# Performance work log

Hardware: AMD Instinct MI355X
Metric: run time of the kernel (lower is better)

Reference implementation:

```python
import jax, jax.numpy as jnp
import numpy as np

NEG = -1e9


def _ln(x, g, b):
    m = x.mean(-1, keepdims=True)
    v = ((x - m) ** 2).mean(-1, keepdims=True)
    return (x - m) / jnp.sqrt(v + 1e-5) * g + b


def _block(single, pair, single_mask, pair_mask,
           pa_ln_g, pa_ln_b, pa_wqkv, pa_wg, pa_wout,
           pt_ln_g, pt_ln_b, pt_w1, pt_b1, pt_w2, pt_b2,
           sa_ln_g, sa_ln_b, sa_wq, sa_wkv, sa_wb, sa_wout,
           st_ln_g, st_ln_b, st_w1, st_b1, st_w2, st_b2):
    B, L, _, D = pair.shape
    H = sa_wb.shape[1]
    hd = D // H
    scale = 1.0 / jnp.sqrt(jnp.asarray(hd, dtype=pair.dtype))
    # ---- PairUpdate: PairAttention over L*L pseudo-tokens ----
    z = _ln(pair, pa_ln_g, pa_ln_b)                       # [B,L,L,D]
    N = L * L
    qkv = (z @ pa_wqkv).reshape(B, N, 3, H, hd)
    q = qkv[:, :, 0].transpose(0, 2, 1, 3)                # [B,H,N,hd]
    k = qkv[:, :, 1].transpose(0, 2, 1, 3)
    v = qkv[:, :, 2].transpose(0, 2, 1, 3)
    attn = jnp.einsum('bhid,bhjd->bhij', q, k) * scale    # [B,H,N,N]
    pm = pair_mask.reshape(B, 1, N)
    m = pm[:, :, :, None] * pm[:, :, None, :]             # [B,1,N,N]
    attn = jnp.where(m > 0, attn, NEG)
    attn = jax.nn.softmax(attn, axis=-1)
    out = jnp.einsum('bhij,bhjd->bhid', attn, v)          # [B,H,N,hd]
    out = out.transpose(0, 2, 1, 3).reshape(B, L, L, D)
    g = jax.nn.sigmoid(z @ pa_wg)
    out = (out @ pa_wout) * g * pair_mask[..., None]
    pair = pair + out
    t = _ln(pair, pt_ln_g, pt_ln_b)
    t = jax.nn.relu(t @ pt_w1 + pt_b1) @ pt_w2 + pt_b2
    pair = pair + t * pair_mask[..., None]
    # ---- SingleUpdate: AttentionPairBias ----
    s = _ln(single, sa_ln_g, sa_ln_b)                     # [B,L,D]
    q = (s @ sa_wq).reshape(B, L, H, hd)
    kv = (s @ sa_wkv).reshape(B, L, 2, H, hd)
    k2, v2 = kv[:, :, 0], kv[:, :, 1]
    attn = jnp.einsum('bihd,bjhd->bhij', q, k2) * scale   # [B,H,L,L]
    bias = (pair @ sa_wb).transpose(0, 3, 1, 2)           # [B,H,L,L]
    attn = attn + bias
    sm = single_mask[:, None, None, :]
    attn = jnp.where(sm > 0, attn, NEG)
    attn = jax.nn.softmax(attn, axis=-1)
    out = jnp.einsum('bhij,bjhd->bihd', attn, v2).reshape(B, L, D)
    single = single + (out @ sa_wout) * single_mask[..., None]
    # single transition
    t = _ln(single, st_ln_g, st_ln_b)
    t = jax.nn.relu(t @ st_w1 + st_b1) @ st_w2 + st_b2
    single = single + t * single_mask[..., None]
    return single, pair


def setup_inputs() -> dict:
    key = jax.random.key(0)
    B, L, D, H = 1, 64, 144, 8
    ks = iter(jax.random.split(key, 40))
    def nrm(shape, scale=0.02):
        return jax.random.normal(next(ks), shape, dtype=jnp.float32) * scale
    sm = jnp.ones((B, L), jnp.float32).at[:, L - 8:].set(0.0)
    pm = sm[:, :, None] * sm[:, None, :]
    return dict(
        single=jax.random.normal(next(ks), (B, L, D), jnp.float32),
        pair=jax.random.normal(next(ks), (B, L, L, D), jnp.float32),
        single_mask=sm,
        pair_mask=pm,
        pa_ln_g=jnp.ones((D,), jnp.float32), pa_ln_b=jnp.zeros((D,), jnp.float32),
        pa_wqkv=nrm((D, 3 * D)), pa_wg=nrm((D, D)), pa_wout=nrm((D, D)),
        pt_ln_g=jnp.ones((D,), jnp.float32), pt_ln_b=jnp.zeros((D,), jnp.float32),
        pt_w1=nrm((D, 4 * D)), pt_b1=jnp.zeros((4 * D,), jnp.float32),
        pt_w2=nrm((4 * D, D)), pt_b2=jnp.zeros((D,), jnp.float32),
        sa_ln_g=jnp.ones((D,), jnp.float32), sa_ln_b=jnp.zeros((D,), jnp.float32),
        sa_wq=nrm((D, D)), sa_wkv=nrm((D, 2 * D)), sa_wb=nrm((D, H)), sa_wout=nrm((D, D)),
        st_ln_g=jnp.ones((D,), jnp.float32), st_ln_b=jnp.zeros((D,), jnp.float32),
        st_w1=nrm((D, 4 * D)), st_b1=jnp.zeros((4 * D,), jnp.float32),
        st_w2=nrm((4 * D, D)), st_b2=jnp.zeros((D,), jnp.float32),
    )


def reference(single, pair, single_mask, pair_mask,
              pa_ln_g, pa_ln_b, pa_wqkv, pa_wg, pa_wout,
              pt_ln_g, pt_ln_b, pt_w1, pt_b1, pt_w2, pt_b2,
              sa_ln_g, sa_ln_b, sa_wq, sa_wkv, sa_wb, sa_wout,
              st_ln_g, st_ln_b, st_w1, st_b1, st_w2, st_b2):
    return _block(single, pair, single_mask, pair_mask,
                  pa_ln_g, pa_ln_b, pa_wqkv, pa_wg, pa_wout,
                  pt_ln_g, pt_ln_b, pt_w1, pt_b1, pt_w2, pt_b2,
                  sa_ln_g, sa_ln_b, sa_wq, sa_wkv, sa_wb, sa_wout,
                  st_ln_g, st_ln_b, st_w1, st_b1, st_w2, st_b2)
```

## Files before the change

kernel.cpp:

```cpp
#include <hip/hip_runtime.h>
#include <hip/hip_bf16.h>

typedef __hip_bfloat16 bf16;
typedef __attribute__((ext_vector_type(8))) short short8;
typedef __attribute__((ext_vector_type(16))) float floatx16;

__device__ __forceinline__ float tof(bf16 x){ return __bfloat162float(x); }
__device__ __forceinline__ float bflo(unsigned u){ return __uint_as_float(u<<16); }
__device__ __forceinline__ float bfhi(unsigned u){ return __uint_as_float(u & 0xFFFF0000u); }
__device__ __forceinline__ float ldT(const void* p, long i, bool isf){
  return isf ? ((const float*)p)[i] : tof(((const bf16*)p)[i]);
}
__device__ __forceinline__ void stT(void* p, long i, bool isf, float v){
  if (isf) ((float*)p)[i] = v; else ((bf16*)p)[i] = __float2bfloat16(v);
}

#define LL 64
#define DD 144
#define NN 4096
#define HH 8
#define HDIM 18
#define SCALE 0.23570226039551584f
#define LOG2E 1.4426950408889634f

__global__ __launch_bounds__(256) void prep_weights(const unsigned* __restrict__ smaskw,
    int* __restrict__ dflag,
    const void* __restrict__ wqkv, const void* __restrict__ wg,
    const void* __restrict__ wout, const void* __restrict__ w1, const void* __restrict__ w2,
    const void* __restrict__ swq, const void* __restrict__ swkv,
    const void* __restrict__ swout, const void* __restrict__ sw1, const void* __restrict__ sw2,
    bf16* __restrict__ F1, bf16* __restrict__ Fout, bf16* __restrict__ Fw1,
    bf16* __restrict__ Fw2, bf16* __restrict__ Fs1, bf16* __restrict__ Wtswout,
    bf16* __restrict__ Wtst1, bf16* __restrict__ Wtst2){
  bool isf = (smaskw[0] == 0x3F800000u);
  if (blockIdx.x==0 && threadIdx.x==0) dflag[0] = isf ? 4 : 2;
  long t = (long)blockIdx.x*256 + threadIdx.x;
  if (t < 82944){
    int j=t&7, lane=(int)((t>>3)&63); long tk=t>>9; int ks=tk%9, tile=tk/9;
    int col=tile*32+(lane&31); int k=ks*16+(lane>>5)*8+j;
    float v = (col<432)? ldT(wqkv,(long)k*432+col,isf) : ldT(wg,(long)k*144+(col-432),isf);
    F1[t]=__float2bfloat16(v); return;
  } t -= 82944;
  if (t < 23040){
    int j=t&7, lane=(int)((t>>3)&63); long tk=t>>9; int ks=tk%9, tile=tk/9;
    int col=tile*32+(lane&31); if (col>143) col=143;
    int k=ks*16+(lane>>5)*8+j;
    Fout[t]=__float2bfloat16(ldT(wout,(long)k*144+col,isf)); return;
  } t -= 23040;
  if (t < 82944){
    int j=t&7, lane=(int)((t>>3)&63); long tk=t>>9; int ks=tk%9, tile=tk/9;
    int col=tile*32+(lane&31); int k=ks*16+(lane>>5)*8+j;
    Fw1[t]=__float2bfloat16(ldT(w1,(long)k*576+col,isf)); return;
  } t -= 82944;
  if (t < 92160){
    int j=t&7, lane=(int)((t>>3)&63); long tk=t>>9; int ks=tk%36, tile=tk/36;
    int col=tile*32+(lane&31); if (col>143) col=143;
    int k=ks*16+(lane>>5)*8+j;
    Fw2[t]=__float2bfloat16(ldT(w2,(long)k*144+col,isf)); return;
  } t -= 92160;
  if (t < 64512){
    int j=t&7, lane=(int)((t>>3)&63); long tk=t>>9; int ks=tk%9, tile=tk/9;
    int col=tile*32+(lane&31); if (col>431) col=431;
    int k=ks*16+(lane>>5)*8+j;
    float v = (col<144)? ldT(swq,(long)k*144+col,isf) : ldT(swkv,(long)k*288+(col-144),isf);
    Fs1[t]=__float2bfloat16(v); return;
  } t -= 64512;
  if (t < 20736){ int c=t/144,k=t-(long)c*144; Wtswout[t]=__float2bfloat16(ldT(swout,(long)k*144+c,isf)); return; }
  t -= 20736;
  if (t < 82944){ int c=t/144,k=t-(long)c*144; Wtst1[t]=__float2bfloat16(ldT(sw1,(long)k*576+c,isf)); return; }
  t -= 82944;
  if (t < 82944){ int c=t/576,k=t-(long)c*576; Wtst2[t]=__float2bfloat16(ldT(sw2,(long)k*144+c,isf)); return; }
}

__global__ __launch_bounds__(256) void ln_rows(const int* __restrict__ df,
    const void* __restrict__ xv,
    const void* __restrict__ gv, const void* __restrict__ bv,
    bf16* __restrict__ out){
  bool isf = (df[0]==4);
  int row = blockIdx.x*4 + (threadIdx.x>>6);
  int lane = threadIdx.x & 63;
  long base = (long)row*DD;
  float e0 = ldT(xv,base+lane,isf);
  float e1 = ldT(xv,base+lane+64,isf);
  float e2 = (lane<16) ? ldT(xv,base+lane+128,isf) : 0.f;
  float s = e0+e1+e2;
  #pragma unroll
  for (int o=32;o;o>>=1) s += __shfl_xor(s,o);
  float mean = s*(1.f/144.f);
  float d0=e0-mean, d1=e1-mean, d2=(lane<16)?(e2-mean):0.f;
  float v = d0*d0+d1*d1+d2*d2;
  #pragma unroll
  for (int o=32;o;o>>=1) v += __shfl_xor(v,o);
  float rstd = rsqrtf(v*(1.f/144.f)+1e-5f);
  out[base+lane]    = __float2bfloat16(d0*rstd*ldT(gv,lane,isf)    + ldT(bv,lane,isf));
  out[base+lane+64] = __float2bfloat16(d1*rstd*ldT(gv,lane+64,isf) + ldT(bv,lane+64,isf));
  if (lane<16)
    out[base+lane+128] = __float2bfloat16(d2*rstd*ldT(gv,lane+128,isf) + ldT(bv,lane+128,isf));
}

__global__ __launch_bounds__(256) void gemm_fused1(const int* __restrict__ df,
    const bf16* __restrict__ z, const bf16* __restrict__ F1,
    const void* __restrict__ pmask,
    bf16* __restrict__ Qb, bf16* __restrict__ Kf, bf16* __restrict__ Vf,
    bf16* __restrict__ gbuf){
  __shared__ short As[64*152];
  bool isf = df[0]==4;
  int row0 = blockIdx.y*64, col0 = blockIdx.x*64;
  int tid=threadIdx.x, lane=tid&63, l31=lane&31, w=tid>>6, wr=w>>1, wc=w&1;
  int g=(lane>>5)*8;
  for (int t=tid; t<64*72; t+=256){
    int m = t/72, dw = t%72;
    ((unsigned*)As)[m*76+dw] = ((const unsigned*)(z + (size_t)(row0+m)*144))[dw];
  }
  __syncthreads();
  int tile = blockIdx.x*2 + wc;
  const short8* wf = (const short8*)F1;
  floatx16 acc;
  #pragma unroll
  for (int i=0;i<16;i++) acc[i]=0.f;
  #pragma unroll
  for (int ks=0; ks<9; ks++){
    short8 af = *(const short8*)&As[(l31+32*wr)*152 + ks*16 + g];
    acc = __builtin_amdgcn_mfma_f32_32x32x16_bf16(af, wf[(tile*9+ks)*64+lane], acc, 0,0,0);
  }
  int col = col0 + wc*32 + l31;
  #pragma unroll
  for (int r=0;r<16;r++){
    int row = row0 + 32*wr + (r&3)+8*(r>>2)+4*(lane>>5);
    if (col < 144){
      int hh = col/18, d = col - hh*18;
      Qb[((size_t)hh*NN+row)*32 + d] = __float2bfloat16(acc[r]*(SCALE*LOG2E));
    } else if (col < 288){
      int c2 = col-144, hh = c2/18, d = c2 - hh*18;
      int f = d>>4, rem = d&15, gs = rem>>3, j = rem&7;
      Kf[((((size_t)hh*128 + (row>>5))*2 + f)*64 + gs*32 + (row&31))*8 + j]
        = __float2bfloat16(acc[r]);
    } else if (col < 432){
      int c2 = col-288, hh = c2/18, d = c2 - hh*18;
      float pm = (ldT(pmask,row,isf)>0.f)?1.f:0.f;
      int kin = row&31, f = kin>>4, k15 = kin&15;
      int gs = (k15>>2)&1, j = (k15&3) | (((k15>>3)&1)<<2);
      Vf[((((size_t)hh*128 + (row>>5))*2 + f)*64 + gs*32 + d)*8 + j]
        = __float2bfloat16(acc[r]*pm);
    } else {
      int c2 = col-432;
      float gt = 1.f/(1.f+__expf(fminf(-acc[r],30.f)));
      gbuf[(size_t)row*DD+c2] = __float2bfloat16(gt);
    }
  }
  if (blockIdx.x==0){
    for (int t=threadIdx.x; t<64*8*7; t+=256){
      int n = row0 + t/56; int rem = t%56; int hh = rem/7, dw = rem%7 + 9;
      ((unsigned*)(Qb + ((size_t)hh*NN+n)*32))[dw] = 0;
    }
    for (int t=threadIdx.x; t<64*8; t+=256){
      int n = row0 + (t>>3), hh = t&7;
      float pm = (ldT(pmask,n,isf)>0.f)?1.f:0.f;
      int kin = n&31, f = kin>>4, k15 = kin&15;
      int gs = (k15>>2)&1, j = (k15&3) | (((k15>>3)&1)<<2);
      Vf[((((size_t)hh*128 + (n>>5))*2 + f)*64 + gs*32 + 18)*8 + j] = __float2bfloat16(pm);
    }
  }
}

__global__ __launch_bounds__(256) void pair_attn_mfma(const int* __restrict__ df,
    const bf16* __restrict__ Qb, const bf16* __restrict__ Kf,
    const bf16* __restrict__ Vf, bf16* __restrict__ aob){
  __shared__ float Comb[4][32][20];
  int h = blockIdx.x >> 7, qt = blockIdx.x & 127;
  int tid = threadIdx.x;
  int w = tid >> 6, lane = tid & 63;
  int l31 = lane & 31, gsel = lane>>5;

  const unsigned* qp = (const unsigned*)(Qb + ((size_t)h*NN + qt*32 + l31)*32);
  short8 qf0, qf1;
  #pragma unroll
  for (int j=0;j<4;j++) ((unsigned*)&qf0)[j] = qp[gsel*4+j];
  #pragma unroll
  for (int j=0;j<4;j++) ((unsigned*)&qf1)[j] = qp[8+gsel*4+j];

  floatx16 o;
  #pragma unroll
  for (int i=0;i<16;i++) o[i]=0.f;

  const short8* kf8 = (const short8*)Kf + (size_t)h*16384;
  const short8* vf8 = (const short8*)Vf + (size_t)h*16384;
  int c0 = w*32;

  short8 af0 = kf8[(c0*2+0)*64 + lane];
  short8 af1 = kf8[(c0*2+1)*64 + lane];
  short8 av0 = vf8[(c0*2+0)*64 + lane];
  short8 av1 = vf8[(c0*2+1)*64 + lane];

  for (int cc=0; cc<32; cc++){
    int cn = c0 + (cc<31 ? cc+1 : 31);
    short8 naf0 = kf8[(cn*2+0)*64 + lane];
    short8 naf1 = kf8[(cn*2+1)*64 + lane];
    short8 nav0 = vf8[(cn*2+0)*64 + lane];
    short8 nav1 = vf8[(cn*2+1)*64 + lane];

    floatx16 s;
    #pragma unroll
    for (int i=0;i<16;i++) s[i]=0.f;
    s = __builtin_amdgcn_mfma_f32_32x32x16_bf16(af0, qf0, s, 0,0,0);
    s = __builtin_amdgcn_mfma_f32_32x32x16_bf16(af1, qf1, s, 0,0,0);

    short8 P1, P2;
    #pragma unroll
    for (int j=0;j<4;j++){
      unsigned e0 = __float_as_uint(__builtin_amdgcn_exp2f(s[2*j]));
      unsigned e1 = __float_as_uint(__builtin_amdgcn_exp2f(s[2*j+1]));
      ((unsigned*)&P1)[j] = (e0>>16) | (e1 & 0xFFFF0000u);
      unsigned e2 = __float_as_uint(__builtin_amdgcn_exp2f(s[8+2*j]));
      unsigned e3 = __float_as_uint(__builtin_amdgcn_exp2f(s[9+2*j]));
      ((unsigned*)&P2)[j] = (e2>>16) | (e3 & 0xFFFF0000u);
    }

    o = __builtin_amdgcn_mfma_f32_32x32x16_bf16(av0, P1, o, 0,0,0);
    o = __builtin_amdgcn_mfma_f32_32x32x16_bf16(av1, P2, o, 0,0,0);

    af0=naf0; af1=naf1; av0=nav0; av1=nav1;
  }

  #pragma unroll
  for (int r=0;r<16;r++){
    int d = (r&3) + 8*(r>>2) + 4*gsel;
    if (d < 20) Comb[w][l31][d] = o[r];
  }
  __syncthreads();
  for (int t=tid; t<32*HDIM; t+=256){
    int q = t/HDIM, d = t-q*HDIM;
    float num = Comb[0][q][d]+Comb[1][q][d]+Comb[2][q][d]+Comb[3][q][d];
    float den = Comb[0][q][18]+Comb[1][q][18]+Comb[2][q][18]+Comb[3][q][18];
    aob[(size_t)(qt*32+q)*DD + h*HDIM + d] = __float2bfloat16(num/fmaxf(den,1e-20f));
  }
}

__global__ __launch_bounds__(512) void pair_tail(const int* __restrict__ df,
    const bf16* __restrict__ aob, const bf16* __restrict__ gbuf,
    const void* __restrict__ pairv, const void* __restrict__ pmaskv,
    const bf16* __restrict__ Fout, const void* __restrict__ ptln_g, const void* __restrict__ ptln_b,
    const bf16* __restrict__ Fw1, const void* __restrict__ b1v,
    const bf16* __restrict__ Fw2, const void* __restrict__ b2v,
    const void* __restrict__ wb, void* __restrict__ outP, long outOff,
    float* __restrict__ biasb){
  __shared__ __align__(16) char smem[16384];
  float* p1  = (float*)smem;
  short* ts  = (short*)(smem + 4608);
  short* hh_ = (short*)(smem + 7040);
  float* outv = (float*)(smem + 7040);

  bool isf = df[0]==4;
  int tid=threadIdx.x, lane=tid&63, l31=lane&31, gsel=lane>>5, g=gsel*8;
  int w=tid>>6;
  int lrow = l31 & 7;
  int r0 = blockIdx.x*8;
  const short8* foutf = (const short8*)Fout;
  const short8* fw1f  = (const short8*)Fw1;
  const short8* fw2f  = (const short8*)Fw2;

  for (int t=tid; t<8*72; t+=512){
    int m=t/72, dw=t%72;
    ((unsigned*)ts)[m*76+dw] = ((const unsigned*)(aob + (size_t)(r0+m)*144))[dw];
  }
  __syncthreads();

  for (int tile=w; tile<5; tile+=8){
    int c0=tile*32;
    floatx16 acc;
    #pragma unroll
    for (int i=0;i<16;i++) acc[i]=0.f;
    #pragma unroll
    for (int ks=0; ks<9; ks++){
      short8 af = *(const short8*)&ts[lrow*152 + ks*16 + g];
      acc = __builtin_amdgcn_mfma_f32_32x32x16_bf16(af, foutf[(tile*9+ks)*64+lane], acc, 0,0,0);
    }
    if (c0+l31 < 144){
      #pragma unroll
      for (int r=0;r<16;r++){
        int row=(r&3)+8*(r>>2)+4*gsel;
        if (row<8) p1[row*144 + c0+l31] = acc[r];
      }
    }
  }
  __syncthreads();
  for (int t=tid; t<8*144; t+=512){
    int row=t/144; int col=t-row*144;
    long gidx=(long)(r0+row)*144 + col;
    float pm = (ldT(pmaskv, r0+row, isf)>0.f)?1.f:0.f;
    p1[t] = ldT(pairv,gidx,isf) + p1[t]*tof(gbuf[gidx])*pm;
  }
  __syncthreads();
  if (w < 8){
    int rr = w;
    float e0=p1[rr*144+lane], e1=p1[rr*144+lane+64], e2=(lane<16)?p1[rr*144+lane+128]:0.f;
    float s=e0+e1+e2;
    #pragma unroll
    for (int o=32;o;o>>=1) s += __shfl_xor(s,o);
    float mean=s*(1.f/144.f);
    float d0=e0-mean, d1=e1-mean, d2=(lane<16)?(e2-mean):0.f;
    float v=d0*d0+d1*d1+d2*d2;
    #pragma unroll
    for (int o=32;o;o>>=1) v += __shfl_xor(v,o);
    float rstd=rsqrtf(v*(1.f/144.f)+1e-5f);
    bf16 h0 = __float2bfloat16(d0*rstd*ldT(ptln_g,lane,isf)    + ldT(ptln_b,lane,isf));
    bf16 h1 = __float2bfloat16(d1*rstd*ldT(ptln_g,lane+64,isf) + ldT(ptln_b,lane+64,isf));
    ts[rr*152+lane]    = *reinterpret_cast<short*>(&h0);
    ts[rr*152+lane+64] = *reinterpret_cast<short*>(&h1);
    if (lane<16){
      bf16 h2 = __float2bfloat16(d2*rstd*ldT(ptln_g,lane+128,isf) + ldT(ptln_b,lane+128,isf));
      ts[rr*152+lane+128] = *reinterpret_cast<short*>(&h2);
    }
  }
  __syncthreads();
  for (int tile=w; tile<18; tile+=8){
    int c0=tile*32, colB=c0+l31;
    floatx16 acc;
    #pragma unroll
    for (int i=0;i<16;i++) acc[i]=0.f;
    #pragma unroll
    for (int ks=0; ks<9; ks++){
      short8 af = *(const short8*)&ts[lrow*152 + ks*16 + g];
      acc = __builtin_amdgcn_mfma_f32_32x32x16_bf16(af, fw1f[(tile*9+ks)*64+lane], acc, 0,0,0);
    }
    float bb = ldT(b1v,colB,isf);
    #pragma unroll
    for (int r=0;r<16;r++){
      int row=(r&3)+8*(r>>2)+4*gsel;
      if (row<8){
        bf16 hv = __float2bfloat16(fmaxf(acc[r]+bb,0.f));
        hh_[row*584 + colB] = *reinterpret_cast<short*>(&hv);
      }
    }
  }
  __syncthreads();
  floatx16 fin; int fc0 = -1;
  for (int tile=w; tile<5; tile+=8){
    int c0=tile*32;
    int colB=c0+l31; if (colB>143) colB=143;
    floatx16 acc;
    #pragma unroll
    for (int i=0;i<16;i++) acc[i]=0.f;
    #pragma unroll
    for (int ks=0; ks<36; ks++){
      short8 af = *(const short8*)&hh_[lrow*584 + ks*16 + g];
      acc = __builtin_amdgcn_mfma_f32_32x32x16_bf16(af, fw2f[(tile*36+ks)*64+lane], acc, 0,0,0);
    }
    float bb = ldT(b2v,colB,isf);
    #pragma unroll
    for (int r=0;r<16;r++){
      int row=(r&3)+8*(r>>2)+4*gsel;
      float val = 0.f;
      if (row<8){
        float pm = (ldT(pmaskv, r0+row, isf)>0.f)?1.f:0.f;
        val = p1[row*144 + colB] + (acc[r]+bb)*pm;
        if (c0+l31 < 144)
          stT(outP, outOff + (long)(r0+row)*144 + c0+l31, isf, val);
      }
      fin[r]=val;
    }
    fc0 = c0;
  }
  __syncthreads();
  if (fc0 >= 0 && fc0+l31 < 144){
    #pragma unroll
    for (int r=0;r<16;r++){
      int row=(r&3)+8*(r>>2)+4*gsel;
      if (row<8) outv[row*144 + fc0+l31] = fin[r];
    }
  }
  __syncthreads();
  {
    int n = tid>>3, hb = tid&7;
    if (n < 8){
      float acc=0.f;
      #pragma unroll 4
      for (int k=0;k<144;k++) acc += outv[n*144+k]*ldT(wb,k*8+hb,isf);
      biasb[(size_t)(r0+n)*8+hb]=acc;
    }
  }
}

__global__ __launch_bounds__(256) void gemm_s1(const int* __restrict__ df,
    const void* __restrict__ single, const void* __restrict__ g, const void* __restrict__ b,
    const bf16* __restrict__ Fs1,
    bf16* __restrict__ q_sb, bf16* __restrict__ kv_sb){
  __shared__ short As[64*152];
  bool isf = df[0]==4;
  int tid=threadIdx.x, lane=tid&63, l31=lane&31, w=tid>>6, wr=w>>1, wc=w&1;
  int gg=(lane>>5)*8;
  for (int rr=w; rr<64; rr+=4){
    long base=(long)rr*DD;
    float e0=ldT(single,base+lane,isf), e1=ldT(single,base+lane+64,isf);
    float e2=(lane<16)?ldT(single,base+lane+128,isf):0.f;
    float s=e0+e1+e2;
    #pragma unroll
    for (int o=32;o;o>>=1) s += __shfl_xor(s,o);
    float mean=s*(1.f/144.f);
    float d0=e0-mean, d1=e1-mean, d2=(lane<16)?(e2-mean):0.f;
    float v=d0*d0+d1*d1+d2*d2;
    #pragma unroll
    for (int o=32;o;o>>=1) v += __shfl_xor(v,o);
    float rstd=rsqrtf(v*(1.f/144.f)+1e-5f);
    bf16 h0=__float2bfloat16(d0*rstd*ldT(g,lane,isf)+ldT(b,lane,isf));
    bf16 h1=__float2bfloat16(d1*rstd*ldT(g,lane+64,isf)+ldT(b,lane+64,isf));
    As[rr*152+lane]=*reinterpret_cast<short*>(&h0);
    As[rr*152+lane+64]=*reinterpret_cast<short*>(&h1);
    if (lane<16){
      bf16 h2=__float2bfloat16(d2*rstd*ldT(g,lane+128,isf)+ldT(b,lane+128,isf));
      As[rr*152+lane+128]=*reinterpret_cast<short*>(&h2);
    }
  }
  __syncthreads();
  int tile = blockIdx.x*2 + wc;
  const short8* wf = (const short8*)Fs1;
  floatx16 acc;
  #pragma unroll
  for (int i=0;i<16;i++) acc[i]=0.f;
  #pragma unroll
  for (int ks=0; ks<9; ks++){
    short8 af = *(const short8*)&As[(l31+32*wr)*152 + ks*16 + gg];
    acc = __builtin_amdgcn_mfma_f32_32x32x16_bf16(af, wf[(tile*9+ks)*64+lane], acc, 0,0,0);
  }
  int col = tile*32 + l31;
  if (col < 432){
    #pragma unroll
    for (int r=0;r<16;r++){
      int row = 32*wr + (r&3)+8*(r>>2)+4*(lane>>5);
      if (col<144) q_sb[(size_t)row*DD+col] = __float2bfloat16(acc[r]);
      else kv_sb[(size_t)row*288+(col-144)] = __float2bfloat16(acc[r]);
    }
  }
}

__global__ __launch_bounds__(256) void single_tail(const int* __restrict__ df,
    const void* __restrict__ single, const bf16* __restrict__ q_sb,
    const bf16* __restrict__ kv_sb, const float* __restrict__ biasb,
    const void* __restrict__ smask, const bf16* __restrict__ Wtswout,
    const void* __restrict__ stln_g, const void* __restrict__ stln_b,
    const bf16* __restrict__ Wtst1, const void* __restrict__ st_b1,
    const bf16* __restrict__ Wtst2, const void* __restrict__ st_b2,
    void* __restrict__ outS){
  bool isf = df[0]==4;
  __shared__ short kvs[64*288];
  __shared__ float pexp[8][64];
  __shared__ float tot[8];
  __shared__ float bb[512];
  __shared__ float qs[DD], as_[DD], s1[DD], tss[DD], hs[576];
  int n = blockIdx.x, tid = threadIdx.x;
  for (int t=tid; t<64*144; t+=256)
    ((unsigned*)kvs)[t] = ((const unsigned*)kv_sb)[t];
  if (tid<DD) qs[tid] = tof(q_sb[(size_t)n*DD+tid]);
  for (int t=tid; t<512; t+=256) bb[t] = biasb[(size_t)n*512 + t];
  __syncthreads();
  #pragma unroll
  for (int pp=0; pp<2; pp++){
    int pi = tid + pp*256;
    int h = pi>>6, j = pi&63;
    const short* kr = &kvs[j*288 + h*HDIM];
    float s=0.f;
    #pragma unroll
    for (int d=0;d<HDIM;d++){
      unsigned u = ((unsigned)(unsigned short)kr[d])<<16;
      s += qs[h*HDIM+d]*__uint_as_float(u);
    }
    s = fminf(s*SCALE + bb[j*8+h], 30.f);
    pexp[h][j] = (ldT(smask,j,isf)>0.f) ? __expf(s) : 0.f;
  }
  __syncthreads();
  if (tid<8){
    float t2=0.f;
    #pragma unroll 4
    for (int j=0;j<64;j++) t2 += pexp[tid][j];
    tot[tid] = fmaxf(t2,1e-20f);
  }
  __syncthreads();
  if (tid<DD){
    int h = tid/HDIM, d = tid - h*HDIM;
    float acc=0.f;
    #pragma unroll 4
    for (int j=0;j<64;j++){
      unsigned u = ((unsigned)(unsigned short)kvs[j*288 + 144 + h*HDIM + d])<<16;
      acc += pexp[h][j]*__uint_as_float(u);
    }
    as_[tid] = acc/tot[h];
  }
  __syncthreads();
  float sm = ldT(smask,n,isf);
  if (tid<DD){
    const unsigned* wr = (const unsigned*)(Wtswout + (size_t)tid*DD);
    float a=0.f;
    #pragma unroll 4
    for (int kw=0; kw<72; kw++){ unsigned u = wr[kw]; a += as_[2*kw]*bflo(u) + as_[2*kw+1]*bfhi(u); }
    s1[tid] = ldT(single,(long)n*DD+tid,isf) + a*sm;
  }
  __syncthreads();
  __shared__ float mr[2];
  if (tid < 64){
    float e0 = s1[tid], e1 = s1[tid+64], e2 = (tid<16)?s1[tid+128]:0.f;
    float s = e0+e1+e2;
    #pragma unroll
    for (int o=32;o;o>>=1) s += __shfl_xor(s,o);
    float mean = s*(1.f/144.f);
    float d0=e0-mean, d1=e1-mean, d2=(tid<16)?(e2-mean):0.f;
    float v = d0*d0+d1*d1+d2*d2;
    #pragma unroll
    for (int o=32;o;o>>=1) v += __shfl_xor(v,o);
    if (tid==0){ mr[0]=mean; mr[1]=rsqrtf(v*(1.f/144.f)+1e-5f); }
  }
  __syncthreads();
  if (tid<DD) tss[tid] = (s1[tid]-mr[0])*mr[1]*ldT(stln_g,tid,isf) + ldT(stln_b,tid,isf);
  __syncthreads();
  for (int c=tid;c<576;c+=256){
    const unsigned* wr = (const unsigned*)(Wtst1 + (size_t)c*DD);
    float a=ldT(st_b1,c,isf);
    #pragma unroll 4
    for (int kw=0; kw<72; kw++){ unsigned u = wr[kw]; a += tss[2*kw]*bflo(u) + tss[2*kw+1]*bfhi(u); }
    hs[c]=fmaxf(a,0.f);
  }
  __syncthreads();
  if (tid<DD){
    const unsigned* wr = (const unsigned*)(Wtst2 + (size_t)tid*576);
    float a=ldT(st_b2,tid,isf);
    #pragma unroll 4
    for (int kw=0; kw<288; kw++){ unsigned u = wr[kw]; a += hs[2*kw]*bflo(u) + hs[2*kw+1]*bfhi(u); }
    stT(outS,(long)n*DD+tid,isf, s1[tid] + a*sm);
  }
}

extern "C" void kernel_launch(void* const* d_in, const int* in_sizes, int n_in,
                              void* d_out, int out_size, void* d_ws, size_t ws_size,
                              hipStream_t stream) {
  char* wsb = (char*)d_ws;
  int*   dflag = (int*)wsb;
  bf16*  F1     = (bf16*)(wsb + 16);
  bf16*  Fout   = F1 + 82944;
  bf16*  Fw1    = Fout + 23040;
  bf16*  Fw2    = Fw1 + 82944;
  bf16*  Fs1    = Fw2 + 92160;
  bf16*  Wtswout= Fs1 + 64512;
  bf16*  Wtst1  = Wtswout + 20736;
  bf16*  Wtst2  = Wtst1 + 82944;
  bf16*  Qb   = Wtst2 + 82944;
  bf16*  Kf   = Qb + (size_t)HH*NN*32;
  bf16*  Vf   = Kf + (size_t)HH*131072;
  bf16*  gbuf = Vf + (size_t)HH*131072;
  bf16*  z    = gbuf + (size_t)NN*DD;
  bf16*  aob  = z + (size_t)NN*DD;
  float* biasb= (float*)(aob + (size_t)NN*DD);
  bf16*  q_sb = (bf16*)(biasb + NN*8);
  bf16*  kv_sb= q_sb + LL*DD;

  const long OUTP_OFF = (long)LL*DD;

  prep_weights<<<2079,256,0,stream>>>((const unsigned*)d_in[2], dflag,
      d_in[6], d_in[7], d_in[8], d_in[11], d_in[13],
      d_in[17], d_in[18], d_in[20], d_in[23], d_in[25],
      F1, Fout, Fw1, Fw2, Fs1, Wtswout, Wtst1, Wtst2);

  ln_rows<<<NN/4,256,0,stream>>>(dflag, d_in[1], d_in[4], d_in[5], z);
  gemm_fused1<<<dim3(9,64),256,0,stream>>>(dflag, z, F1, d_in[3], Qb, Kf, Vf, gbuf);
  pair_attn_mfma<<<1024,256,0,stream>>>(dflag, Qb, Kf, Vf, aob);
  pair_tail<<<512,512,0,stream>>>(dflag, aob, gbuf, d_in[1], d_in[3],
                                  Fout, d_in[9], d_in[10], Fw1, d_in[12],
                                  Fw2, d_in[14], d_in[19], d_out, OUTP_OFF, biasb);

  gemm_s1<<<dim3(7,1),256,0,stream>>>(dflag, d_in[0], d_in[15], d_in[16], Fs1, q_sb, kv_sb);
  single_tail<<<LL,256,0,stream>>>(dflag, d_in[0], q_sb, kv_sb, biasb, d_in[2],
                                   Wtswout, d_in[21], d_in[22], Wtst1, d_in[24],
                                   Wtst2, d_in[26], d_out);
  (void)in_sizes; (void)n_in; (void)out_size; (void)ws_size;
}
```

Baseline: 239.6 us.

## Fuse pair LayerNorm into QKV GEMM, fuse single path, reorder attention blocks

Folds the pair LayerNorm into the QKV/gate GEMM's shared-memory staging, so the separate ln_rows launch and the z buffer round-trip disappear. The single-track LN+QKV GEMM is merged into the single tail kernel: each of the 64 blocks recomputes the full 64-row projection locally instead of reading from a separate launch. Pair attention block indexing now interleaves heads across consecutive blocks, and MFMA sections are wrapped with s_setprio. The fusions save two launches and a global round-trip but add redundant work: the 9 column blocks each redo the LN on their rows, and every single-track block recomputes the same GEMM.

```diff
diff --git a/kernel.cpp b/kernel.cpp
--- a/kernel.cpp
+++ b/kernel.cpp
@@ -72,34 +72,9 @@
   if (t < 82944){ int c=t/576,k=t-(long)c*576; Wtst2[t]=__float2bfloat16(ldT(sw2,(long)k*144+c,isf)); return; }
 }
 
-__global__ __launch_bounds__(256) void ln_rows(const int* __restrict__ df,
-    const void* __restrict__ xv,
-    const void* __restrict__ gv, const void* __restrict__ bv,
-    bf16* __restrict__ out){
-  bool isf = (df[0]==4);
-  int row = blockIdx.x*4 + (threadIdx.x>>6);
-  int lane = threadIdx.x & 63;
-  long base = (long)row*DD;
-  float e0 = ldT(xv,base+lane,isf);
-  float e1 = ldT(xv,base+lane+64,isf);
-  float e2 = (lane<16) ? ldT(xv,base+lane+128,isf) : 0.f;
-  float s = e0+e1+e2;
-  #pragma unroll
-  for (int o=32;o;o>>=1) s += __shfl_xor(s,o);
-  float mean = s*(1.f/144.f);
-  float d0=e0-mean, d1=e1-mean, d2=(lane<16)?(e2-mean):0.f;
-  float v = d0*d0+d1*d1+d2*d2;
-  #pragma unroll
-  for (int o=32;o;o>>=1) v += __shfl_xor(v,o);
-  float rstd = rsqrtf(v*(1.f/144.f)+1e-5f);
-  out[base+lane]    = __float2bfloat16(d0*rstd*ldT(gv,lane,isf)    + ldT(bv,lane,isf));
-  out[base+lane+64] = __float2bfloat16(d1*rstd*ldT(gv,lane+64,isf) + ldT(bv,lane+64,isf));
-  if (lane<16)
-    out[base+lane+128] = __float2bfloat16(d2*rstd*ldT(gv,lane+128,isf) + ldT(bv,lane+128,isf));
-}
-
 __global__ __launch_bounds__(256) void gemm_fused1(const int* __restrict__ df,
-    const bf16* __restrict__ z, const bf16* __restrict__ F1,
+    const void* __restrict__ pairv, const void* __restrict__ lng, const void* __restrict__ lnb,
+    const bf16* __restrict__ F1,
     const void* __restrict__ pmask,
     bf16* __restrict__ Qb, bf16* __restrict__ Kf, bf16* __restrict__ Vf,
     bf16* __restrict__ gbuf){
@@ -108,9 +83,27 @@
   int row0 = blockIdx.y*64, col0 = blockIdx.x*64;
   int tid=threadIdx.x, lane=tid&63, l31=lane&31, w=tid>>6, wr=w>>1, wc=w&1;
   int g=(lane>>5)*8;
-  for (int t=tid; t<64*72; t+=256){
-    int m = t/72, dw = t%72;
-    ((unsigned*)As)[m*76+dw] = ((const unsigned*)(z + (size_t)(row0+m)*144))[dw];
+  for (int rr=w; rr<64; rr+=4){
+    long base=(long)(row0+rr)*DD;
+    float e0=ldT(pairv,base+lane,isf), e1=ldT(pairv,base+lane+64,isf);
+    float e2=(lane<16)?ldT(pairv,base+lane+128,isf):0.f;
+    float s=e0+e1+e2;
+    #pragma unroll
+    for (int o=32;o;o>>=1) s += __shfl_xor(s,o);
+    float mean=s*(1.f/144.f);
+    float d0=e0-mean, d1=e1-mean, d2=(lane<16)?(e2-mean):0.f;
+    float v=d0*d0+d1*d1+d2*d2;
+    #pragma unroll
+    for (int o=32;o;o>>=1) v += __shfl_xor(v,o);
+    float rstd=rsqrtf(v*(1.f/144.f)+1e-5f);
+    bf16 h0=__float2bfloat16(d0*rstd*ldT(lng,lane,isf)+ldT(lnb,lane,isf));
+    bf16 h1=__float2bfloat16(d1*rstd*ldT(lng,lane+64,isf)+ldT(lnb,lane+64,isf));
+    As[rr*152+lane]=*reinterpret_cast<short*>(&h0);
+    As[rr*152+lane+64]=*reinterpret_cast<short*>(&h1);
+    if (lane<16){
+      bf16 h2=__float2bfloat16(d2*rstd*ldT(lng,lane+128,isf)+ldT(lnb,lane+128,isf));
+      As[rr*152+lane+128]=*reinterpret_cast<short*>(&h2);
+    }
   }
   __syncthreads();
   int tile = blockIdx.x*2 + wc;
@@ -167,7 +160,7 @@
     const bf16* __restrict__ Qb, const bf16* __restrict__ Kf,
     const bf16* __restrict__ Vf, bf16* __restrict__ aob){
   __shared__ float Comb[4][32][20];
-  int h = blockIdx.x >> 7, qt = blockIdx.x & 127;
+  int h = blockIdx.x & 7, qt = blockIdx.x >> 3;
   int tid = threadIdx.x;
   int w = tid >> 6, lane = tid & 63;
   int l31 = lane & 31, gsel = lane>>5;
@@ -202,8 +195,10 @@
     floatx16 s;
     #pragma unroll
     for (int i=0;i<16;i++) s[i]=0.f;
+    __builtin_amdgcn_s_setprio(1);
     s = __builtin_amdgcn_mfma_f32_32x32x16_bf16(af0, qf0, s, 0,0,0);
     s = __builtin_amdgcn_mfma_f32_32x32x16_bf16(af1, qf1, s, 0,0,0);
+    __builtin_amdgcn_s_setprio(0);
 
     short8 P1, P2;
     #pragma unroll
@@ -216,8 +211,10 @@
       ((unsigned*)&P2)[j] = (e2>>16) | (e3 & 0xFFFF0000u);
     }
 
+    __builtin_amdgcn_s_setprio(1);
     o = __builtin_amdgcn_mfma_f32_32x32x16_bf16(av0, P1, o, 0,0,0);
     o = __builtin_amdgcn_mfma_f32_32x32x16_bf16(av1, P2, o, 0,0,0);
+    __builtin_amdgcn_s_setprio(0);
 
     af0=naf0; af1=naf1; av0=nav0; av1=nav1;
   }
@@ -381,78 +378,78 @@
   }
 }
 
-__global__ __launch_bounds__(256) void gemm_s1(const int* __restrict__ df,
-    const void* __restrict__ single, const void* __restrict__ g, const void* __restrict__ b,
-    const bf16* __restrict__ Fs1,
-    bf16* __restrict__ q_sb, bf16* __restrict__ kv_sb){
-  __shared__ short As[64*152];
-  bool isf = df[0]==4;
-  int tid=threadIdx.x, lane=tid&63, l31=lane&31, w=tid>>6, wr=w>>1, wc=w&1;
-  int gg=(lane>>5)*8;
-  for (int rr=w; rr<64; rr+=4){
-    long base=(long)rr*DD;
-    float e0=ldT(single,base+lane,isf), e1=ldT(single,base+lane+64,isf);
-    float e2=(lane<16)?ldT(single,base+lane+128,isf):0.f;
-    float s=e0+e1+e2;
-    #pragma unroll
-    for (int o=32;o;o>>=1) s += __shfl_xor(s,o);
-    float mean=s*(1.f/144.f);
-    float d0=e0-mean, d1=e1-mean, d2=(lane<16)?(e2-mean):0.f;
-    float v=d0*d0+d1*d1+d2*d2;
-    #pragma unroll
-    for (int o=32;o;o>>=1) v += __shfl_xor(v,o);
-    float rstd=rsqrtf(v*(1.f/144.f)+1e-5f);
-    bf16 h0=__float2bfloat16(d0*rstd*ldT(g,lane,isf)+ldT(b,lane,isf));
-    bf16 h1=__float2bfloat16(d1*rstd*ldT(g,lane+64,isf)+ldT(b,lane+64,isf));
-    As[rr*152+lane]=*reinterpret_cast<short*>(&h0);
-    As[rr*152+lane+64]=*reinterpret_cast<short*>(&h1);
-    if (lane<16){
-      bf16 h2=__float2bfloat16(d2*rstd*ldT(g,lane+128,isf)+ldT(b,lane+128,isf));
-      As[rr*152+lane+128]=*reinterpret_cast<short*>(&h2);
-    }
-  }
-  __syncthreads();
-  int tile = blockIdx.x*2 + wc;
-  const short8* wf = (const short8*)Fs1;
-  floatx16 acc;
-  #pragma unroll
-  for (int i=0;i<16;i++) acc[i]=0.f;
-  #pragma unroll
-  for (int ks=0; ks<9; ks++){
-    short8 af = *(const short8*)&As[(l31+32*wr)*152 + ks*16 + gg];
-    acc = __builtin_amdgcn_mfma_f32_32x32x16_bf16(af, wf[(tile*9+ks)*64+lane], acc, 0,0,0);
-  }
-  int col = tile*32 + l31;
-  if (col < 432){
-    #pragma unroll
-    for (int r=0;r<16;r++){
-      int row = 32*wr + (r&3)+8*(r>>2)+4*(lane>>5);
-      if (col<144) q_sb[(size_t)row*DD+col] = __float2bfloat16(acc[r]);
-      else kv_sb[(size_t)row*288+(col-144)] = __float2bfloat16(acc[r]);
-    }
-  }
-}
-
-__global__ __launch_bounds__(256) void single_tail(const int* __restrict__ df,
-    const void* __restrict__ single, const bf16* __restrict__ q_sb,
-    const bf16* __restrict__ kv_sb, const float* __restrict__ biasb,
+__global__ __launch_bounds__(256) void single_fused(const int* __restrict__ df,
+    const void* __restrict__ single, const void* __restrict__ sag, const void* __restrict__ sab,
+    const bf16* __restrict__ Fs1, const float* __restrict__ biasb,
     const void* __restrict__ smask, const bf16* __restrict__ Wtswout,
     const void* __restrict__ stln_g, const void* __restrict__ stln_b,
     const bf16* __restrict__ Wtst1, const void* __restrict__ st_b1,
     const bf16* __restrict__ Wtst2, const void* __restrict__ st_b2,
     void* __restrict__ outS){
   bool isf = df[0]==4;
+  __shared__ short As2[64*152];
   __shared__ short kvs[64*288];
   __shared__ float pexp[8][64];
   __shared__ float tot[8];
   __shared__ float bb[512];
   __shared__ float qs[DD], as_[DD], s1[DD], tss[DD], hs[576];
+  __shared__ float mr[2];
   int n = blockIdx.x, tid = threadIdx.x;
-  for (int t=tid; t<64*144; t+=256)
-    ((unsigned*)kvs)[t] = ((const unsigned*)kv_sb)[t];
-  if (tid<DD) qs[tid] = tof(q_sb[(size_t)n*DD+tid]);
+  int lane=tid&63, l31=lane&31, w=tid>>6;
+  int gg=(lane>>5)*8;
+
+  for (int rr=w; rr<64; rr+=4){
+    long base=(long)rr*DD;
+    float e0=ldT(single,base+lane,isf), e1=ldT(single,base+lane+64,isf);
+    float e2=(lane<16)?ldT(single,base+lane+128,isf):0.f;
+    float s=e0+e1+e2;
+    #pragma unroll
+    for (int o=32;o;o>>=1) s += __shfl_xor(s,o);
+    float mean=s*(1.f/144.f);
+    float d0=e0-mean, d1=e1-mean, d2=(lane<16)?(e2-mean):0.f;
+    float v=d0*d0+d1*d1+d2*d2;
+    #pragma unroll
+    for (int o=32;o;o>>=1) v += __shfl_xor(v,o);
+    float rstd=rsqrtf(v*(1.f/144.f)+1e-5f);
+    bf16 h0=__float2bfloat16(d0*rstd*ldT(sag,lane,isf)+ldT(sab,lane,isf));
+    bf16 h1=__float2bfloat16(d1*rstd*ldT(sag,lane+64,isf)+ldT(sab,lane+64,isf));
+    As2[rr*152+lane]=*reinterpret_cast<short*>(&h0);
+    As2[rr*152+lane+64]=*reinterpret_cast<short*>(&h1);
+    if (lane<16){
+      bf16 h2=__float2bfloat16(d2*rstd*ldT(sag,lane+128,isf)+ldT(sab,lane+128,isf));
+      As2[rr*152+lane+128]=*reinterpret_cast<short*>(&h2);
+    }
+  }
   for (int t=tid; t<512; t+=256) bb[t] = biasb[(size_t)n*512 + t];
   __syncthreads();
+
+  const short8* wf = (const short8*)Fs1;
+  for (int jj=w; jj<28; jj+=4){
+    int tile=jj>>1, rt=jj&1;
+    floatx16 acc;
+    #pragma unroll
+    for (int i=0;i<16;i++) acc[i]=0.f;
+    #pragma unroll
+    for (int ks=0; ks<9; ks++){
+      short8 af = *(const short8*)&As2[(l31+32*rt)*152 + ks*16 + gg];
+      acc = __builtin_amdgcn_mfma_f32_32x32x16_bf16(af, wf[(tile*9+ks)*64+lane], acc, 0,0,0);
+    }
+    int col = tile*32 + l31;
+    if (col < 432){
+      #pragma unroll
+      for (int r=0;r<16;r++){
+        int row = 32*rt + (r&3)+8*(r>>2)+4*(lane>>5);
+        if (col < 144){
+          if (row == n) qs[col] = acc[r];
+        } else {
+          bf16 hv = __float2bfloat16(acc[r]);
+          kvs[row*288 + (col-144)] = *reinterpret_cast<short*>(&hv);
+        }
+      }
+    }
+  }
+  __syncthreads();
+
   #pragma unroll
   for (int pp=0; pp<2; pp++){
     int pi = tid + pp*256;
@@ -495,7 +492,6 @@
     s1[tid] = ldT(single,(long)n*DD+tid,isf) + a*sm;
   }
   __syncthreads();
-  __shared__ float mr[2];
   if (tid < 64){
     float e0 = s1[tid], e1 = s1[tid+64], e2 = (tid<16)?s1[tid+128]:0.f;
     float s = e0+e1+e2;
@@ -545,11 +541,8 @@
   bf16*  Kf   = Qb + (size_t)HH*NN*32;
   bf16*  Vf   = Kf + (size_t)HH*131072;
   bf16*  gbuf = Vf + (size_t)HH*131072;
-  bf16*  z    = gbuf + (size_t)NN*DD;
-  bf16*  aob  = z + (size_t)NN*DD;
+  bf16*  aob  = gbuf + (size_t)NN*DD;
   float* biasb= (float*)(aob + (size_t)NN*DD);
-  bf16*  q_sb = (bf16*)(biasb + NN*8);
-  bf16*  kv_sb= q_sb + LL*DD;
 
   const long OUTP_OFF = (long)LL*DD;
 
@@ -558,16 +551,15 @@
       d_in[17], d_in[18], d_in[20], d_in[23], d_in[25],
       F1, Fout, Fw1, Fw2, Fs1, Wtswout, Wtst1, Wtst2);
 
-  ln_rows<<<NN/4,256,0,stream>>>(dflag, d_in[1], d_in[4], d_in[5], z);
-  gemm_fused1<<<dim3(9,64),256,0,stream>>>(dflag, z, F1, d_in[3], Qb, Kf, Vf, gbuf);
+  gemm_fused1<<<dim3(9,64),256,0,stream>>>(dflag, d_in[1], d_in[4], d_in[5], F1, d_in[3],
+                                           Qb, Kf, Vf, gbuf);
   pair_attn_mfma<<<1024,256,0,stream>>>(dflag, Qb, Kf, Vf, aob);
   pair_tail<<<512,512,0,stream>>>(dflag, aob, gbuf, d_in[1], d_in[3],
                                   Fout, d_in[9], d_in[10], Fw1, d_in[12],
                                   Fw2, d_in[14], d_in[19], d_out, OUTP_OFF, biasb);
 
-  gemm_s1<<<dim3(7,1),256,0,stream>>>(dflag, d_in[0], d_in[15], d_in[16], Fs1, q_sb, kv_sb);
-  single_tail<<<LL,256,0,stream>>>(dflag, d_in[0], q_sb, kv_sb, biasb, d_in[2],
-                                   Wtswout, d_in[21], d_in[22], Wtst1, d_in[24],
-                                   Wtst2, d_in[26], d_out);
+  single_fused<<<LL,256,0,stream>>>(dflag, d_in[0], d_in[15], d_in[16], Fs1, biasb,
+                                    d_in[2], Wtswout, d_in[21], d_in[22], Wtst1, d_in[24],
+                                    Wtst2, d_in[26], d_out);
   (void)in_sizes; (void)n_in; (void)out_size; (void)ws_size;
 }
```

Result: slower. 256.0 us (+6.8%).
